# Optimization experiments

Hardware: AMD Instinct MI355X
Metric: run time of the kernel (lower is better)

Reference implementation:

```python
import jax, jax.numpy as jnp
import numpy as np

EMB_DIM = 256
NUM_EMB = 1024
COMMITMENT = 0.25
DECAY = 0.9
EPS = 1e-5
B, H, W = 32, 64, 64


def setup_inputs() -> dict:
    key = jax.random.key(0)
    k1, k2 = jax.random.split(key)
    x = jax.random.normal(k1, (B, EMB_DIM, H, W), dtype=jnp.float32)
    embed = jax.random.normal(k2, (EMB_DIM, NUM_EMB), dtype=jnp.float32)
    cluster_size = jnp.zeros((NUM_EMB,), dtype=jnp.float32)
    ema_embed = embed  # registered as embed.clone() in the torch module
    return {"x": x, "embed": embed, "cluster_size": cluster_size, "ema_embed": ema_embed}


def reference(x, embed, cluster_size, ema_embed):
    # x: [B, C, H, W] -> [B, H, W, C]
    xp = jnp.transpose(x, (0, 2, 3, 1))
    flat = xp.reshape(-1, EMB_DIM)  # [N, D]
    # squared-distance matrix [N, K]
    dist = (jnp.sum(flat * flat, axis=1, keepdims=True)
            - 2.0 * (flat @ embed)
            + jnp.sum(embed * embed, axis=0, keepdims=True))
    embed_idx_flat = jnp.argmin(dist, axis=1)  # [N]
    embed_idx = embed_idx_flat.reshape(xp.shape[:-1])  # [B, H, W]
    quantize = embed.T[embed_idx]  # gather -> [B, H, W, D]

    # training-mode EMA codebook update (buffer updates in torch)
    ref_count = jax.ops.segment_sum(jnp.ones_like(embed_idx_flat, dtype=flat.dtype),
                                    embed_idx_flat, num_segments=NUM_EMB)  # [K]
    new_cluster_size = cluster_size * DECAY + (1.0 - DECAY) * ref_count
    n = jnp.sum(new_cluster_size)
    smoothing = n * ((new_cluster_size + EPS) / (n + new_cluster_size * EPS))
    # dw = flatten^T @ onehot, computed as a segment sum: [K, D] -> [D, K]
    dw = jax.ops.segment_sum(flat, embed_idx_flat, num_segments=NUM_EMB).T
    new_ema_embed = ema_embed * DECAY + (1.0 - DECAY) * dw
    new_embed = new_ema_embed / smoothing[None, :]

    e_latent_loss = jnp.mean((jax.lax.stop_gradient(quantize) - xp) ** 2)
    loss = COMMITMENT * e_latent_loss
    # straight-through estimator
    quantize_st = xp + jax.lax.stop_gradient(quantize - xp)
    out = jnp.transpose(quantize_st, (0, 3, 1, 2))  # [B, C, H, W]
    return out, loss, embed_idx, new_embed, new_cluster_size, new_ema_embed
```

## Files before the change

kernel.cpp:

```cpp
#include <hip/hip_runtime.h>
#include <cfloat>
#include <cstdint>

typedef unsigned short u16;

#define NTOK   131072
#define DIM    256
#define NCODE  1024
#define HW     4096
#define PLANE  1048576
#define DECAYF 0.9f
#define EPSF   1e-5f

#define O_OUT     0
#define O_LOSS    33554432
#define O_IDX     33554433
#define O_NEWEMB  33685505
#define O_NCS     33947649
#define O_NEE     33948673

#define P_XS      0
#define P_V1      16777216
#define P_V2      17825792
#define P_KK      18874368
#define P_VF      19922944
#define P_DW      20054016
#define P_BT      22151168
#define P_ENORM64 22413312
#define P_HLIST   22415360

#define WS_ENORM  0
#define WS_CNT    1024
#define WS_LOSS   2048
#define WS_RC     2049
#define WS_RC2    2050
#define WS_LIST   2051
#define WS_SMOOTH 34819

#define REF_CAP 32768
#define DELTA   0.25f
#define MARGIN  0.03f
#define RT      16

typedef __attribute__((ext_vector_type(8))) short bf16x8;
typedef __attribute__((ext_vector_type(4))) float f32x4;

__device__ __forceinline__ u16 bf16_rne(float f) {
    unsigned int u = __float_as_uint(f);
    unsigned int r = u + 0x7FFF + ((u >> 16) & 1);
    return (u16)(r >> 16);
}
__device__ __forceinline__ float bf16_to_f(u16 s) {
    return __uint_as_float(((unsigned int)s) << 16);
}
__device__ __forceinline__ void gload_lds16(const void* g, void* l) {
    __builtin_amdgcn_global_load_lds(
        (const __attribute__((address_space(1))) unsigned int*)g,
        (__attribute__((address_space(3))) unsigned int*)l, 16, 0, 0);
}

__global__ void k_enorm(const float* __restrict__ embed, float* __restrict__ enorm,
                        double* __restrict__ enorm64) {
    int k = blockIdx.x * 256 + threadIdx.x;
    double s = 0.0;
    for (int d = 0; d < DIM; ++d) {
        float e = embed[(size_t)d * NCODE + k];
        s += (double)e * (double)e;
    }
    enorm[k] = (float)s;
    enorm64[k] = s;
}

__global__ __launch_bounds__(256) void k_xs(const float* __restrict__ x,
                                            u16* __restrict__ Xs,
                                            float* __restrict__ loss_acc)
{
    __shared__ float tile[64 * 65];
    __shared__ float red[256];
    const int tid = threadIdx.x;
    const int blk = blockIdx.x;
    const int b = blk >> 8;
    const int dc = (blk >> 6) & 3;
    const int hwc = blk & 63;
    const int d0 = dc * 64, hw0 = hwc * 64;
    const int r = tid >> 2, s = tid & 3;
    float sq = 0.f;
#pragma unroll
    for (int j = 0; j < 4; ++j) {
        float4 v = *(const float4*)&x[(size_t)b * PLANE + (size_t)(d0 + r) * HW + hw0 + s * 16 + j * 4];
        int c = s * 16 + j * 4;
        tile[r * 65 + c + 0] = v.x; tile[r * 65 + c + 1] = v.y;
        tile[r * 65 + c + 2] = v.z; tile[r * 65 + c + 3] = v.w;
        sq = fmaf(v.x, v.x, sq); sq = fmaf(v.y, v.y, sq);
        sq = fmaf(v.z, v.z, sq); sq = fmaf(v.w, v.w, sq);
    }
    __syncthreads();
    const int tk = tid >> 2, dq = tid & 3;
    u16 us[16];
#pragma unroll
    for (int j = 0; j < 16; ++j)
        us[j] = bf16_rne(tile[(dq * 16 + j) * 65 + tk]);
    size_t ob = (size_t)(b * 4096 + hw0 + tk) * 256 + d0 + dq * 16;
    *(uint4*)&Xs[ob]     = *(uint4*)&us[0];
    *(uint4*)&Xs[ob + 8] = *(uint4*)&us[8];
    red[tid] = sq; __syncthreads();
    for (int st = 128; st > 0; st >>= 1) {
        if (tid < st) red[tid] += red[tid + st];
        __syncthreads();
    }
    if (tid == 0) atomicAdd(loss_acc, red[0]);
}

__global__ __launch_bounds__(256) void k_bt(const float* __restrict__ embed, u16* __restrict__ Bt)
{
    const int tile = blockIdx.x;
    const int cc = tile >> 4, kc = tile & 15;
    const int seg = kc >> 3, dbase = (kc & 7) * 32;
    const int tid = threadIdx.x;
#pragma unroll
    for (int g2 = 0; g2 < 2; ++g2) {
        int p = g2 * 256 + tid;
        int n = p >> 2, s = p & 3, lg = (s - n) & 3;
        int code = cc * 128 + n;
        u16 us[8];
#pragma unroll
        for (int e = 0; e < 8; ++e) {
            int d = dbase + lg * 8 + e;
            float E = embed[(size_t)d * NCODE + code];
            u16 hi = bf16_rne(E);
            us[e] = seg ? bf16_rne(E - bf16_to_f(hi)) : hi;
        }
        *(uint4*)&Bt[(size_t)tile * 4096 + (size_t)p * 8] = *(uint4*)&us[0];
    }
}

__global__ __launch_bounds__(256) void k_dist(
    const u16* __restrict__ Xs, const u16* __restrict__ Bt,
    const float* __restrict__ enorm,
    float* __restrict__ pv1, float* __restrict__ pv2, float* __restrict__ pkk)
{
    __shared__ __align__(16) u16 lds[12288];
    const int tid = threadIdx.x;
    const int w = tid >> 6, l = tid & 63;
    const int cc = blockIdx.x >> 10;
    const int n0 = (blockIdx.x & 1023) * 128;
    const int mh = w & 1, nh = w >> 1;
    const int lane15 = l & 15, quad = l >> 4;

    const u16* src[6];
    u16* dst[6];
#pragma unroll
    for (int r = 0; r < 6; ++r) {
        int p = r * 256 + w * 64 + l;
        dst[r] = &lds[(size_t)(r * 256 + w * 64) * 8];
        if (p < 512) {
            int m = p >> 2, s = p & 3, lg = (s - m) & 3;
            src[r] = Xs + (size_t)(n0 + m) * 256 + lg * 8;
        } else {
            int q = p - 512;
            int kcb = (q >> 9) * 8;
            int qq = q & 511;
            src[r] = Bt + (size_t)(cc * 16 + kcb) * 4096 + (size_t)qq * 8;
        }
    }

    f32x4 acc[4][4];
#pragma unroll
    for (int i = 0; i < 4; ++i)
#pragma unroll
        for (int j = 0; j < 4; ++j) acc[i][j] = (f32x4)0.f;

    for (int kc8 = 0; kc8 < 8; ++kc8) {
        __syncthreads();
#pragma unroll
        for (int r = 0; r < 6; ++r) {
            const u16* s = src[r] + (r < 2 ? (size_t)kc8 * 32 : (size_t)kc8 * 4096);
            gload_lds16(s, dst[r]);
        }
        __syncthreads();

        bf16x8 af[4];
#pragma unroll
        for (int mt = 0; mt < 4; ++mt) {
            int m = mh * 64 + mt * 16 + lane15;
            int slot = (quad + m) & 3;
            af[mt] = *(const bf16x8*)&lds[(size_t)(m * 4 + slot) * 8];
        }
#pragma unroll
        for (int seg = 0; seg < 2; ++seg) {
#pragma unroll
            for (int nt = 0; nt < 4; ++nt) {
                int n = nh * 64 + nt * 16 + lane15;
                int slot = (quad + n) & 3;
                bf16x8 bfr = *(const bf16x8*)&lds[(size_t)(512 + seg * 512 + n * 4 + slot) * 8];
#pragma unroll
                for (int mt = 0; mt < 4; ++mt)
                    acc[mt][nt] = __builtin_amdgcn_mfma_f32_16x16x32_bf16(af[mt], bfr, acc[mt][nt], 0, 0, 0);
            }
        }
    }

    float ev[4]; int ec[4];
#pragma unroll
    for (int nt = 0; nt < 4; ++nt) {
        ec[nt] = cc * 128 + nh * 64 + nt * 16 + lane15;
        ev[nt] = enorm[ec[nt]];
    }
    float r1[4][4], r2[4][4]; int rk[4][4];
#pragma unroll
    for (int mt = 0; mt < 4; ++mt)
#pragma unroll
        for (int rg = 0; rg < 4; ++rg) {
            float v1 = FLT_MAX, v2 = FLT_MAX; int k1 = 1 << 30;
#pragma unroll
            for (int nt = 0; nt < 4; ++nt) {
                float d = fmaf(-2.f, acc[mt][nt][rg], ev[nt]);
                if (d < v1) { v2 = v1; v1 = d; k1 = ec[nt]; }
                else v2 = fminf(v2, d);
            }
            r1[mt][rg] = v1; r2[mt][rg] = v2; rk[mt][rg] = k1;
        }
#pragma unroll
    for (int mask = 1; mask <= 8; mask <<= 1) {
#pragma unroll
        for (int mt = 0; mt < 4; ++mt)
#pragma unroll
            for (int rg = 0; rg < 4; ++rg) {
                float ov1 = __shfl_xor(r1[mt][rg], mask);
                float ov2 = __shfl_xor(r2[mt][rg], mask);
                int   ok  = __shfl_xor(rk[mt][rg], mask);
                if (ov1 < r1[mt][rg] || (ov1 == r1[mt][rg] && ok < rk[mt][rg])) {
                    r2[mt][rg] = fminf(r1[mt][rg], ov2);
                    r1[mt][rg] = ov1; rk[mt][rg] = ok;
                } else {
                    r2[mt][rg] = fminf(r2[mt][rg], ov1);
                }
            }
    }
    __syncthreads();
    float* epi = (float*)lds;
    if (lane15 == 0) {
#pragma unroll
        for (int mt = 0; mt < 4; ++mt)
#pragma unroll
            for (int rg = 0; rg < 4; ++rg) {
                int t = mh * 64 + mt * 16 + quad * 4 + rg;
                float* p = &epi[(nh * 128 + t) * 3];
                p[0] = r1[mt][rg]; p[1] = r2[mt][rg]; p[2] = __int_as_float(rk[mt][rg]);
            }
    }
    __syncthreads();
    if (tid < 128) {
        const float* p0 = &epi[tid * 3];
        const float* p1 = &epi[(128 + tid) * 3];
        float v1 = p0[0], v2 = p0[1]; int k1 = __float_as_int(p0[2]);
        float a1 = p1[0], a2 = p1[1]; int ak = __float_as_int(p1[2]);
        if (a1 < v1 || (a1 == v1 && ak < k1)) { v2 = fminf(v1, a2); v1 = a1; k1 = ak; }
        else v2 = fminf(v2, a1);
        size_t o = (size_t)cc * NTOK + n0 + tid;
        pv1[o] = v1; pv2[o] = v2; pkk[o] = (float)k1;
    }
}

__global__ __launch_bounds__(256) void k_amin(
    const float* __restrict__ pv1, const float* __restrict__ pv2, const float* __restrict__ pkk,
    float* __restrict__ out_idx, float* __restrict__ vf, float* __restrict__ loss_acc,
    int* __restrict__ refcnt, int* __restrict__ reflist)
{
    const int n = blockIdx.x * 256 + threadIdx.x;
    float v1 = FLT_MAX, v2 = FLT_MAX; int k1 = 1 << 30;
    for (int cc = 0; cc < 8; ++cc) {
        float a1 = pv1[(size_t)cc * NTOK + n], a2 = pv2[(size_t)cc * NTOK + n];
        int ak = (int)pkk[(size_t)cc * NTOK + n];
        if (a1 < v1 || (a1 == v1 && ak < k1)) { v2 = fminf(v1, a2); v1 = a1; k1 = ak; }
        else v2 = fminf(v2, a1);
    }
    out_idx[n] = (float)k1;
    vf[n] = v1;
    if (v2 - v1 < DELTA) {
        int pos = atomicAdd(refcnt, 1);
        if (pos < REF_CAP) reflist[pos] = n;
    }
    __shared__ float red[256];
    red[threadIdx.x] = v1; __syncthreads();
    for (int s = 128; s > 0; s >>= 1) {
        if (threadIdx.x < s) red[threadIdx.x] += red[threadIdx.x + s];
        __syncthreads();
    }
    if (threadIdx.x == 0) atomicAdd(loss_acc, red[0]);
}

__global__ __launch_bounds__(256) void k_ref32(
    const float* __restrict__ x, const float* __restrict__ embed,
    const float* __restrict__ enorm,
    float* __restrict__ out_idx, const int* __restrict__ refcnt,
    const int* __restrict__ reflist, const float* __restrict__ vf,
    float* __restrict__ loss_acc, int* __restrict__ hardcnt, int* __restrict__ hardlist)
{
    __shared__ float xm2t[DIM][RT + 1];
    __shared__ int toks[RT];
    __shared__ float wv1[4][RT], wv2[4][RT];
    __shared__ int wk1[4][RT];
    const int tid = threadIdx.x;
    const int w = tid >> 6;
    const int cnt = min(*refcnt, REF_CAP);
    for (int base = blockIdx.x * RT; base < cnt; base += gridDim.x * RT) {
        const int nb = min(RT, cnt - base);
        for (int j = 0; j < nb; ++j) {
            int n = reflist[base + j];
            if (tid == 0) toks[j] = n;
            int b = n >> 12, hw = n & 4095;
            xm2t[tid][j] = -2.f * x[(size_t)b * PLANE + (size_t)tid * HW + hw];
        }
        if (nb < RT)
            for (int j = nb; j < RT; ++j) xm2t[tid][j] = 0.f;
        __syncthreads();

        float b1[RT], b2[RT]; int k1[RT];
#pragma unroll
        for (int j = 0; j < RT; ++j) { b1[j] = FLT_MAX; b2[j] = FLT_MAX; k1[j] = 1 << 30; }
#pragma unroll 1
        for (int c = 0; c < 4; ++c) {
            const int k = c * 256 + tid;
            float acc[RT];
#pragma unroll
            for (int j = 0; j < RT; ++j) acc[j] = 0.f;
#pragma unroll 1
            for (int d0 = 0; d0 < DIM; d0 += 8) {
                float er[8];
#pragma unroll
                for (int dd = 0; dd < 8; ++dd)
                    er[dd] = embed[(size_t)(d0 + dd) * NCODE + k];
#pragma unroll
                for (int dd = 0; dd < 8; ++dd)
#pragma unroll
                    for (int j = 0; j < RT; ++j)
                        acc[j] = fmaf(er[dd], xm2t[d0 + dd][j], acc[j]);
            }
            float e2 = enorm[k];
#pragma unroll
            for (int j = 0; j < RT; ++j) {
                float dist = e2 + acc[j];
                if (dist < b1[j]) { b2[j] = b1[j]; b1[j] = dist; k1[j] = k; }
                else b2[j] = fminf(b2[j], dist);
            }
        }

#pragma unroll
        for (int m = 1; m < 64; m <<= 1) {
#pragma unroll
            for (int j = 0; j < RT; ++j) {
                float ov1 = __shfl_xor(b1[j], m);
                float ov2 = __shfl_xor(b2[j], m);
                int   ok  = __shfl_xor(k1[j], m);
                if (ov1 < b1[j] || (ov1 == b1[j] && ok < k1[j])) {
                    b2[j] = fminf(b1[j], ov2); b1[j] = ov1; k1[j] = ok;
                } else {
                    b2[j] = fminf(b2[j], ov1);
                }
            }
        }
        if ((tid & 63) == 0) {
#pragma unroll
            for (int j = 0; j < RT; ++j) { wv1[w][j] = b1[j]; wk1[w][j] = k1[j]; wv2[w][j] = b2[j]; }
        }
        __syncthreads();
        if (tid < nb) {
            float v1 = wv1[0][tid], v2 = wv2[0][tid]; int kk = wk1[0][tid];
#pragma unroll
            for (int wi = 1; wi < 4; ++wi) {
                float a1 = wv1[wi][tid], a2 = wv2[wi][tid]; int ak = wk1[wi][tid];
                if (a1 < v1 || (a1 == v1 && ak < kk)) { v2 = fminf(v1, a2); v1 = a1; kk = ak; }
                else v2 = fminf(v2, a1);
            }
            int n = toks[tid];
            if (v2 - v1 > MARGIN) {
                out_idx[n] = (float)kk;
                atomicAdd(loss_acc, v1 - vf[n]);
            } else {
                int pos = atomicAdd(hardcnt, 1);
                hardlist[pos] = n;
            }
        }
        __syncthreads();
    }
}

__global__ __launch_bounds__(256) void k_ref64(
    const float* __restrict__ x, const float* __restrict__ embed,
    const double* __restrict__ enorm64,
    float* __restrict__ out_idx, const int* __restrict__ hcnt,
    const int* __restrict__ hlist, const float* __restrict__ vf,
    float* __restrict__ loss_acc)
{
    __shared__ float xs[DIM];
    __shared__ double wv[4];
    __shared__ int wk[4];
    const int tid = threadIdx.x;
    const int w = tid >> 6, l = tid & 63;
    const int cnt = min(*hcnt, REF_CAP);
    for (int it = blockIdx.x; it < cnt; it += gridDim.x) {
        const int n = hlist[it];
        const int b = n >> 12, hw = n & 4095;
        xs[tid] = x[(size_t)b * PLANE + (size_t)tid * HW + hw];
        __syncthreads();
        double bv = 1e300; int bk = 1 << 30;
#pragma unroll 1
        for (int c = 0; c < 4; ++c) {
            const int k = c * 256 + tid;
            const float* ep = embed + k;
            double acc = 0.0;
#pragma unroll 8
            for (int d = 0; d < DIM; ++d)
                acc = fma((double)ep[(size_t)d * NCODE], (double)xs[d], acc);
            double dist = enorm64[k] - 2.0 * acc;
            if (dist < bv) { bv = dist; bk = k; }
        }
#pragma unroll
        for (int m = 1; m < 64; m <<= 1) {
            double ov = __shfl_xor(bv, m);
            int ok = __shfl_xor(bk, m);
            if (ov < bv || (ov == bv && ok < bk)) { bv = ov; bk = ok; }
        }
        if (l == 0) { wv[w] = bv; wk[w] = bk; }
        __syncthreads();
        if (tid == 0) {
            double v = wv[0]; int kk = wk[0];
#pragma unroll
            for (int wi = 1; wi < 4; ++wi) {
                if (wv[wi] < v || (wv[wi] == v && wk[wi] < kk)) { v = wv[wi]; kk = wk[wi]; }
            }
            out_idx[n] = (float)kk;
            atomicAdd(loss_acc, (float)(v - (double)vf[n]));
        }
        __syncthreads();
    }
}

__global__ __launch_bounds__(256) void k_cnt(const float* __restrict__ out_idx, float* __restrict__ cnt) {
    const int n = blockIdx.x * 256 + threadIdx.x;
    atomicAdd(&cnt[(int)out_idx[n]], 1.0f);
}

__global__ __launch_bounds__(256) void k_dw(
    const float* __restrict__ x, const float* __restrict__ out_idx, float* __restrict__ part)
{
    __shared__ float tile[NCODE * 9];
    const int tid = threadIdx.x;
    const int slice = blockIdx.x & 31;
    const int chunk = blockIdx.x >> 5;
    const int d0 = slice * 8;
    for (int i = tid; i < NCODE * 9; i += 256) tile[i] = 0.f;
    __syncthreads();
    const int nbeg = chunk * (NTOK / 8);
    for (int t = tid; t < NTOK / 8; t += 256) {
        const int n = nbeg + t;
        const int b = n >> 12, hw = n & 4095;
        const int k = (int)out_idx[n];
        const float* xb = x + (size_t)b * PLANE + hw;
        float* tp = tile + k * 9;
#pragma unroll
        for (int dl = 0; dl < 8; ++dl)
            unsafeAtomicAdd(&tp[dl], xb[(size_t)(d0 + dl) * HW]);
    }
    __syncthreads();
    for (int i = tid; i < 8 * NCODE; i += 256) {
        const int dl = i >> 10, k = i & (NCODE - 1);
        part[((size_t)chunk * DIM + d0 + dl) * NCODE + k] = tile[k * 9 + dl];
    }
}

__global__ __launch_bounds__(1024) void k_fin_cs(
    const float* __restrict__ cs_in, const float* __restrict__ cnt,
    float* __restrict__ out_ncs, float* __restrict__ smooth)
{
    const int k = threadIdx.x;
    float ncs = cs_in[k] * DECAYF + (1.f - DECAYF) * cnt[k];
    out_ncs[k] = ncs;
    __shared__ float red[1024];
    red[k] = ncs; __syncthreads();
    for (int s = 512; s > 0; s >>= 1) {
        if (k < s) red[k] += red[k + s];
        __syncthreads();
    }
    float n = red[0];
    smooth[k] = n * ((ncs + EPSF) / (n + ncs * EPSF));
}

__global__ __launch_bounds__(256) void k_fin_emb(
    const float* __restrict__ ema, const float* __restrict__ part,
    const float* __restrict__ smooth, float* __restrict__ out_ne, float* __restrict__ out_nee)
{
    const int i = blockIdx.x * 256 + threadIdx.x;
    const int k = i & (NCODE - 1);
    float dw = 0.f;
    for (int c = 0; c < 8; ++c) dw += part[(size_t)c * (DIM * NCODE) + i];
    float nee = ema[i] * DECAYF + (1.f - DECAYF) * dw;
    out_nee[i] = nee;
    out_ne[i] = nee / smooth[k];
}

__global__ __launch_bounds__(256) void k_quant(
    const float* __restrict__ embed, const float* __restrict__ out_idx, float* __restrict__ out_q)
{
    const int n = blockIdx.x * 256 + threadIdx.x;
    const int b = n >> 12, hw = n & 4095;
    const int idx = (int)out_idx[n];
    const size_t base = (size_t)b * PLANE + hw;
    for (int d = 0; d < DIM; ++d)
        out_q[base + (size_t)d * HW] = embed[(size_t)d * NCODE + idx];
}

__global__ void k_loss(const float* __restrict__ loss_acc, float* __restrict__ out_loss) {
    out_loss[0] = 0.25f * loss_acc[0] / 33554432.f;
}

extern "C" void kernel_launch(void* const* d_in, const int* in_sizes, int n_in,
                              void* d_out, int out_size, void* d_ws, size_t ws_size,
                              hipStream_t stream) {
    const float* x     = (const float*)d_in[0];
    const float* embed = (const float*)d_in[1];
    const float* csz   = (const float*)d_in[2];
    const float* ema   = (const float*)d_in[3];
    float* out = (float*)d_out;
    float* ws  = (float*)d_ws;

    u16* Xs = (u16*)(out + P_XS);
    u16* Bt = (u16*)(out + P_BT);
    double* enorm64 = (double*)(out + P_ENORM64);

    hipMemsetAsync(ws + WS_CNT, 0, (size_t)(WS_RC2 + 1 - WS_CNT) * sizeof(float), stream);

    k_enorm<<<4, 256, 0, stream>>>(embed, ws + WS_ENORM, enorm64);
    k_xs<<<8192, 256, 0, stream>>>(x, Xs, ws + WS_LOSS);
    k_bt<<<128, 256, 0, stream>>>(embed, Bt);
    k_dist<<<8192, 256, 0, stream>>>(Xs, Bt, ws + WS_ENORM,
                                     out + P_V1, out + P_V2, out + P_KK);
    k_amin<<<NTOK / 256, 256, 0, stream>>>(out + P_V1, out + P_V2, out + P_KK,
                                           out + O_IDX, out + P_VF, ws + WS_LOSS,
                                           (int*)(ws + WS_RC), (int*)(ws + WS_LIST));
    k_ref32<<<2048, 256, 0, stream>>>(x, embed, ws + WS_ENORM, out + O_IDX,
                                      (const int*)(ws + WS_RC), (const int*)(ws + WS_LIST),
                                      out + P_VF, ws + WS_LOSS,
                                      (int*)(ws + WS_RC2), (int*)(out + P_HLIST));
    k_ref64<<<2048, 256, 0, stream>>>(x, embed, enorm64, out + O_IDX,
                                      (const int*)(ws + WS_RC2), (const int*)(out + P_HLIST),
                                      out + P_VF, ws + WS_LOSS);
    k_cnt<<<NTOK / 256, 256, 0, stream>>>(out + O_IDX, ws + WS_CNT);
    k_dw<<<256, 256, 0, stream>>>(x, out + O_IDX, out + P_DW);
    k_fin_cs<<<1, 1024, 0, stream>>>(csz, ws + WS_CNT, out + O_NCS, ws + WS_SMOOTH);
    k_fin_emb<<<1024, 256, 0, stream>>>(ema, out + P_DW, ws + WS_SMOOTH,
                                        out + O_NEWEMB, out + O_NEE);
    k_quant<<<NTOK / 256, 256, 0, stream>>>(embed, out + O_IDX, out + O_OUT);
    k_loss<<<1, 1, 0, stream>>>(ws + WS_LOSS, out + O_LOSS);
}
```

Before: 1.151 ms.

## Double-buffer dist GEMM, XCD-aware block mapping, LDS histogram, split dw and quant

The distance GEMM now double-buffers its LDS tiles, issuing the next K-chunk's global-to-LDS loads before computing the current one, which halves barriers per step. Blocks are remapped so that consecutive blocks on the same XCD share token tiles across code chunks. The count kernel uses a per-block LDS histogram before global atomics, dw is split into 64 token chunks (more blocks, partials stored in the reused Xs region), and the quantize gather splits the dimension four ways for more parallelism. These add LDS use, a larger partial-sum reduction in fin_emb, and depend on Xs being dead by the time it is reused.

```diff
diff --git a/kernel.cpp b/kernel.cpp
--- a/kernel.cpp
+++ b/kernel.cpp
@@ -24,7 +24,6 @@
 #define P_V2      17825792
 #define P_KK      18874368
 #define P_VF      19922944
-#define P_DW      20054016
 #define P_BT      22151168
 #define P_ENORM64 22413312
 #define P_HLIST   22415360
@@ -41,6 +40,7 @@
 #define DELTA   0.25f
 #define MARGIN  0.03f
 #define RT      16
+#define DWC     64
 
 typedef __attribute__((ext_vector_type(8))) short bf16x8;
 typedef __attribute__((ext_vector_type(4))) float f32x4;
@@ -139,52 +139,64 @@
     const float* __restrict__ enorm,
     float* __restrict__ pv1, float* __restrict__ pv2, float* __restrict__ pkk)
 {
-    __shared__ __align__(16) u16 lds[12288];
+    __shared__ __align__(16) u16 lds[24576];
     const int tid = threadIdx.x;
     const int w = tid >> 6, l = tid & 63;
-    const int cc = blockIdx.x >> 10;
-    const int n0 = (blockIdx.x & 1023) * 128;
+    const int xcd = blockIdx.x & 7;
+    const int q = blockIdx.x >> 3;
+    const int cc = q & 7;
+    const int n0 = ((q >> 3) * 8 + xcd) * 128;
     const int mh = w & 1, nh = w >> 1;
     const int lane15 = l & 15, quad = l >> 4;
 
     const u16* src[6];
-    u16* dst[6];
+    int dstoff[6];
 #pragma unroll
     for (int r = 0; r < 6; ++r) {
         int p = r * 256 + w * 64 + l;
-        dst[r] = &lds[(size_t)(r * 256 + w * 64) * 8];
+        dstoff[r] = (r * 256 + w * 64) * 8;
         if (p < 512) {
             int m = p >> 2, s = p & 3, lg = (s - m) & 3;
             src[r] = Xs + (size_t)(n0 + m) * 256 + lg * 8;
         } else {
-            int q = p - 512;
-            int kcb = (q >> 9) * 8;
-            int qq = q & 511;
+            int qq2 = p - 512;
+            int kcb = (qq2 >> 9) * 8;
+            int qq = qq2 & 511;
             src[r] = Bt + (size_t)(cc * 16 + kcb) * 4096 + (size_t)qq * 8;
         }
     }
 
+#define STAGE_K(kc8_, buf_) do {                                              \
+    _Pragma("unroll")                                                         \
+    for (int r_ = 0; r_ < 6; ++r_) {                                          \
+        const u16* s_ = src[r_] + (r_ < 2 ? (size_t)(kc8_) * 32               \
+                                          : (size_t)(kc8_) * 4096);           \
+        gload_lds16(s_, &lds[(buf_) * 12288 + dstoff[r_]]);                   \
+    } } while (0)
+
     f32x4 acc[4][4];
 #pragma unroll
     for (int i = 0; i < 4; ++i)
 #pragma unroll
         for (int j = 0; j < 4; ++j) acc[i][j] = (f32x4)0.f;
 
+    STAGE_K(0, 0);
+
+#pragma unroll 1
     for (int kc8 = 0; kc8 < 8; ++kc8) {
-        __syncthreads();
-#pragma unroll
-        for (int r = 0; r < 6; ++r) {
-            const u16* s = src[r] + (r < 2 ? (size_t)kc8 * 32 : (size_t)kc8 * 4096);
-            gload_lds16(s, dst[r]);
-        }
-        __syncthreads();
-
+        asm volatile("s_waitcnt vmcnt(0)" ::: "memory");
+        __builtin_amdgcn_s_barrier();
+        asm volatile("" ::: "memory");
+
+        if (kc8 < 7) STAGE_K(kc8 + 1, (kc8 + 1) & 1);
+
+        const u16* buf = &lds[(kc8 & 1) * 12288];
         bf16x8 af[4];
 #pragma unroll
         for (int mt = 0; mt < 4; ++mt) {
             int m = mh * 64 + mt * 16 + lane15;
             int slot = (quad + m) & 3;
-            af[mt] = *(const bf16x8*)&lds[(size_t)(m * 4 + slot) * 8];
+            af[mt] = *(const bf16x8*)&buf[(size_t)(m * 4 + slot) * 8];
         }
 #pragma unroll
         for (int seg = 0; seg < 2; ++seg) {
@@ -192,13 +204,14 @@
             for (int nt = 0; nt < 4; ++nt) {
                 int n = nh * 64 + nt * 16 + lane15;
                 int slot = (quad + n) & 3;
-                bf16x8 bfr = *(const bf16x8*)&lds[(size_t)(512 + seg * 512 + n * 4 + slot) * 8];
+                bf16x8 bfr = *(const bf16x8*)&buf[(size_t)(512 + seg * 512 + n * 4 + slot) * 8];
 #pragma unroll
                 for (int mt = 0; mt < 4; ++mt)
                     acc[mt][nt] = __builtin_amdgcn_mfma_f32_16x16x32_bf16(af[mt], bfr, acc[mt][nt], 0, 0, 0);
             }
         }
     }
+#undef STAGE_K
 
     float ev[4]; int ec[4];
 #pragma unroll
@@ -438,8 +451,19 @@
 }
 
 __global__ __launch_bounds__(256) void k_cnt(const float* __restrict__ out_idx, float* __restrict__ cnt) {
-    const int n = blockIdx.x * 256 + threadIdx.x;
-    atomicAdd(&cnt[(int)out_idx[n]], 1.0f);
+    __shared__ float h[NCODE];
+    const int tid = threadIdx.x;
+    for (int i = tid; i < NCODE; i += 256) h[i] = 0.f;
+    __syncthreads();
+    const int base = blockIdx.x * 2048;
+#pragma unroll
+    for (int t = 0; t < 8; ++t)
+        unsafeAtomicAdd(&h[(int)out_idx[base + t * 256 + tid]], 1.0f);
+    __syncthreads();
+    for (int i = tid; i < NCODE; i += 256) {
+        float v = h[i];
+        if (v != 0.f) atomicAdd(&cnt[i], v);
+    }
 }
 
 __global__ __launch_bounds__(256) void k_dw(
@@ -452,8 +476,8 @@
     const int d0 = slice * 8;
     for (int i = tid; i < NCODE * 9; i += 256) tile[i] = 0.f;
     __syncthreads();
-    const int nbeg = chunk * (NTOK / 8);
-    for (int t = tid; t < NTOK / 8; t += 256) {
+    const int nbeg = chunk * (NTOK / DWC);
+    for (int t = tid; t < NTOK / DWC; t += 256) {
         const int n = nbeg + t;
         const int b = n >> 12, hw = n & 4095;
         const int k = (int)out_idx[n];
@@ -494,7 +518,7 @@
     const int i = blockIdx.x * 256 + threadIdx.x;
     const int k = i & (NCODE - 1);
     float dw = 0.f;
-    for (int c = 0; c < 8; ++c) dw += part[(size_t)c * (DIM * NCODE) + i];
+    for (int c = 0; c < DWC; ++c) dw += part[(size_t)c * (DIM * NCODE) + i];
     float nee = ema[i] * DECAYF + (1.f - DECAYF) * dw;
     out_nee[i] = nee;
     out_ne[i] = nee / smooth[k];
@@ -503,11 +527,13 @@
 __global__ __launch_bounds__(256) void k_quant(
     const float* __restrict__ embed, const float* __restrict__ out_idx, float* __restrict__ out_q)
 {
-    const int n = blockIdx.x * 256 + threadIdx.x;
+    const int n = (blockIdx.x >> 2) * 256 + threadIdx.x;
+    const int dc = blockIdx.x & 3;
     const int b = n >> 12, hw = n & 4095;
     const int idx = (int)out_idx[n];
     const size_t base = (size_t)b * PLANE + hw;
-    for (int d = 0; d < DIM; ++d)
+    const int dend = dc * 64 + 64;
+    for (int d = dc * 64; d < dend; ++d)
         out_q[base + (size_t)d * HW] = embed[(size_t)d * NCODE + idx];
 }
 
@@ -546,11 +572,11 @@
     k_ref64<<<2048, 256, 0, stream>>>(x, embed, enorm64, out + O_IDX,
                                       (const int*)(ws + WS_RC2), (const int*)(out + P_HLIST),
                                       out + P_VF, ws + WS_LOSS);
-    k_cnt<<<NTOK / 256, 256, 0, stream>>>(out + O_IDX, ws + WS_CNT);
-    k_dw<<<256, 256, 0, stream>>>(x, out + O_IDX, out + P_DW);
+    k_cnt<<<64, 256, 0, stream>>>(out + O_IDX, ws + WS_CNT);
+    k_dw<<<32 * DWC, 256, 0, stream>>>(x, out + O_IDX, out + P_XS);
     k_fin_cs<<<1, 1024, 0, stream>>>(csz, ws + WS_CNT, out + O_NCS, ws + WS_SMOOTH);
-    k_fin_emb<<<1024, 256, 0, stream>>>(ema, out + P_DW, ws + WS_SMOOTH,
+    k_fin_emb<<<1024, 256, 0, stream>>>(ema, out + P_XS, ws + WS_SMOOTH,
                                         out + O_NEWEMB, out + O_NEE);
-    k_quant<<<NTOK / 256, 256, 0, stream>>>(embed, out + O_IDX, out + O_OUT);
+    k_quant<<<NTOK / 256 * 4, 256, 0, stream>>>(embed, out + O_IDX, out + O_OUT);
     k_loss<<<1, 1, 0, stream>>>(ws + WS_LOSS, out + O_LOSS);
 }
```

Result: faster. 1.109 ms (-3.6%).
